# Kernel optimization log

Measured on AMD Instinct MI355X. Metric: run time of the kernel, lower is better.

## Reference

```python
import jax, jax.numpy as jnp
import numpy as np


def _prelu(x, a):
    return jnp.where(x >= 0, x, a * x)


def _conv1x1(x, w, b, a):
    # x: [N,C,H,W], w: [O,C], b: [O] -> PReLU(conv1x1(x))
    y = jnp.einsum('oc,nchw->nohw', w, x) + b[None, :, None, None]
    return _prelu(y, a)


def setup_inputs() -> dict:
    key = jax.random.key(0)
    ks = jax.random.split(key, 8)
    N, C, H, W = 4, 128, 64, 64
    Cr = C // 2  # reduction=2
    sC = 1.0 / np.sqrt(C)
    x = jax.random.normal(ks[0], (N, C, H, W), dtype=jnp.float32)
    w1 = jax.random.normal(ks[1], (Cr, C), dtype=jnp.float32) * sC
    b1 = jnp.zeros((Cr,), dtype=jnp.float32)
    a1 = jnp.asarray(0.25, dtype=jnp.float32)  # PReLU (single shared slope)
    w2 = jax.random.normal(ks[2], (Cr, C), dtype=jnp.float32) * sC
    b2 = jnp.zeros((Cr,), dtype=jnp.float32)
    a2 = jnp.asarray(0.25, dtype=jnp.float32)
    wa = jax.random.normal(ks[3], (C, C), dtype=jnp.float32) * sC
    ba = jnp.zeros((C,), dtype=jnp.float32)
    aa = jnp.asarray(0.25, dtype=jnp.float32)
    return {"x": x, "w1": w1, "b1": b1, "a1": a1,
            "w2": w2, "b2": b2, "a2": a2,
            "wa": wa, "ba": ba, "aa": aa}


def reference(x, w1, b1, a1, w2, b2, a2, wa, ba, aa):
    N, C, H, W = x.shape
    HW = H * W
    e1 = _conv1x1(x, w1, b1, a1).reshape(N, -1, HW)   # [N,Cr,HW]
    e2 = _conv1x1(x, w2, b2, a2).reshape(N, -1, HW)   # [N,Cr,HW]
    asm = _conv1x1(x, wa, ba, aa).reshape(N, C, HW)   # [N,C,HW]
    # ksize=1: per-channel outer products summed over channels == single contraction
    score = jnp.einsum('nci,ncj->nij', e1, e2)        # [N,HW,HW]
    score = jax.nn.softmax(score, axis=2)
    out = jnp.einsum('nij,ncj->nci', score, asm)      # [N,C,HW]
    return out.reshape(N, C, H, W)
```

## Files before the change

kernel.cpp:

```cpp
#include <hip/hip_runtime.h>
#include <hip/hip_bf16.h>
#include <stdint.h>


typedef float   f32x16 __attribute__((ext_vector_type(16)));
typedef __bf16  bf16x8 __attribute__((ext_vector_type(8)));
typedef __bf16  bf16x2 __attribute__((ext_vector_type(2)));
typedef unsigned int u32x4 __attribute__((ext_vector_type(4)));
typedef unsigned int u32x2 __attribute__((ext_vector_type(2)));

#define L2E 1.4426950408889634f

#define Q_OFF   (0u)
#define K_OFF   (2u << 20)
#define V_OFF   (4u << 20)
#define DEN_OFF (8u << 20)
#define WH_OFF  ((8u << 20) + (1u << 19))
#define WL_OFF  (WH_OFF + (1u << 16))
#define OP_OFF  (9u << 20)

__device__ inline unsigned short f2bf(float f) {
  unsigned u = __builtin_bit_cast(unsigned, f);
  return (unsigned short)((u + 0x7FFFu + ((u >> 16) & 1u)) >> 16);
}
__device__ inline float bf2f(unsigned short h) {
  unsigned u = ((unsigned)h) << 16;
  return __builtin_bit_cast(float, u);
}

__device__ inline void gld_lds16(const void* g, void* l) {
  __builtin_amdgcn_global_load_lds(
      (const __attribute__((address_space(1))) unsigned*)g,
      (__attribute__((address_space(3))) unsigned*)l, 16, 0, 0);
}

__global__ void wcast_kernel(const float* __restrict__ w1, const float* __restrict__ w2,
                             const float* __restrict__ wa, char* __restrict__ ws) {
  int idx = blockIdx.x * 256 + threadIdx.x;
  unsigned short* WH = (unsigned short*)(ws + WH_OFF);
  unsigned short* WL = (unsigned short*)(ws + WL_OFF);
#pragma unroll
  for (int r = 0; r < 4; ++r) {
    int i = r * 8192 + idx;
    int oc = i >> 7, c = i & 127;
    float v = oc < 64 ? w1[oc * 128 + c]
            : (oc < 128 ? w2[(oc - 64) * 128 + c] : wa[(oc - 128) * 128 + c]);
    unsigned short h = f2bf(v);
    WH[i] = h;
    WL[i] = f2bf(v - bf2f(h));
  }
}

__global__ __launch_bounds__(256) void conv_kernel(
    const float* __restrict__ x, char* __restrict__ ws,
    const float* __restrict__ b1, const float* __restrict__ a1,
    const float* __restrict__ b2, const float* __restrict__ a2,
    const float* __restrict__ ba, const float* __restrict__ aa) {
  int bid = blockIdx.x;
  int n = bid >> 7, st = bid & 127;
  int sb = st * 32;
  int tid = threadIdx.x;
  int wid = tid >> 6, lane = tid & 63, l31 = lane & 31, hi = lane >> 5;

  __shared__ float xl[128][36];
  __shared__ float tl[2][64][33];

  const float* xb = x + (size_t)n * 128 * 4096;
#pragma unroll
  for (int it = 0; it < 4; ++it) {
    int flat4 = tid + 256 * it;
    int c = flat4 >> 3, s4 = flat4 & 7;
    float4 v = *(const float4*)(xb + (size_t)c * 4096 + sb + s4 * 4);
    *(float4*)&xl[c][s4 * 4] = v;
  }
  __syncthreads();

  const char* WH = ws + WH_OFF;
  const char* WL = ws + WL_OFF;
  int oc0 = wid * 64;

  f32x16 acc[2];
  acc[0] = 0.f; acc[1] = 0.f;
#pragma unroll
  for (int c0 = 0; c0 < 8; ++c0) {
    __bf16 eh[8], el[8];
#pragma unroll
    for (int j = 0; j < 8; ++j) {
      float v = xl[c0 * 16 + hi * 8 + j][l31];
      __bf16 h = (__bf16)v;
      eh[j] = h;
      el[j] = (__bf16)(v - (float)h);
    }
    bf16x8 xh = {eh[0], eh[1], eh[2], eh[3], eh[4], eh[5], eh[6], eh[7]};
    bf16x8 xlo = {el[0], el[1], el[2], el[3], el[4], el[5], el[6], el[7]};
#pragma unroll
    for (int mb = 0; mb < 2; ++mb) {
      size_t wo = (size_t)(oc0 + mb * 32 + l31) * 256 + c0 * 32 + hi * 16;
      bf16x8 wh = *(const bf16x8*)(WH + wo);
      bf16x8 wl = *(const bf16x8*)(WL + wo);
      acc[mb] = __builtin_amdgcn_mfma_f32_32x32x16_bf16(wh, xh, acc[mb], 0, 0, 0);
      acc[mb] = __builtin_amdgcn_mfma_f32_32x32x16_bf16(wh, xlo, acc[mb], 0, 0, 0);
      acc[mb] = __builtin_amdgcn_mfma_f32_32x32x16_bf16(wl, xh, acc[mb], 0, 0, 0);
    }
  }

  char* Qw = ws + Q_OFF + (size_t)n * (4096 * 64 * 2);
  char* Kw = ws + K_OFF + (size_t)n * (4096 * 64 * 2);
  unsigned short* Vw = (unsigned short*)(ws + V_OFF) + (size_t)n * 128 * 4096;

  if (wid < 2) {
    const float* bb = wid ? b2 : b1;
    float slope = wid ? a2[0] : a1[0];
    float scl = wid ? 1.0f : L2E;
#pragma unroll
    for (int mb = 0; mb < 2; ++mb)
#pragma unroll
      for (int reg = 0; reg < 16; ++reg) {
        int row = mb * 32 + (reg & 3) + 8 * (reg >> 2) + 4 * hi;
        float y = acc[mb][reg] + bb[row];
        y = fmaxf(y, 0.f) + slope * fminf(y, 0.f);
        tl[wid][row][l31] = y * scl;
      }
  } else {
    float slope = aa[0];
#pragma unroll
    for (int mb = 0; mb < 2; ++mb)
#pragma unroll
      for (int reg = 0; reg < 16; ++reg) {
        int dv = (wid - 2) * 64 + mb * 32 + (reg & 3) + 8 * (reg >> 2) + 4 * hi;
        float y = acc[mb][reg] + ba[dv];
        y = fmaxf(y, 0.f) + slope * fminf(y, 0.f);
        Vw[(size_t)dv * 4096 + sb + l31] = f2bf(y);
      }
  }
  __syncthreads();
  if (wid < 2) {
    char* Og = wid ? Kw : Qw;
#pragma unroll
    for (int it = 0; it < 4; ++it) {
      int sl = (lane >> 3) + it * 8;
      unsigned short u[8];
#pragma unroll
      for (int i = 0; i < 8; ++i) u[i] = f2bf(tl[wid][(lane & 7) * 8 + i][sl]);
      u32x4 pv;
      pv.x = ((unsigned)u[1] << 16) | u[0]; pv.y = ((unsigned)u[3] << 16) | u[2];
      pv.z = ((unsigned)u[5] << 16) | u[4]; pv.w = ((unsigned)u[7] << 16) | u[6];
      *(u32x4*)(Og + (size_t)(sb + sl) * 128 + (lane & 7) * 16) = pv;
    }
  }
}

__global__ __launch_bounds__(256, 4) void attn_kernel(char* __restrict__ ws) {
  int bid = blockIdx.x;
  int split = bid & 7;
  int qt = (bid >> 3) & 31;
  int batch = bid >> 8;
  int tid = threadIdx.x;
  int wid = tid >> 6, lane = tid & 63, l31 = lane & 31, hi = lane >> 5;

  const char* Qb = ws + Q_OFF + (size_t)batch * (4096 * 64 * 2);
  const char* Kb = ws + K_OFF + (size_t)batch * (4096 * 64 * 2);
  const char* Vb = ws + V_OFF + (size_t)batch * (128 * 4096 * 2);

  __shared__ char kbuf[2][32 * 128];
  __shared__ char vbuf[2][128 * 64];

  int q0 = qt * 128 + wid * 32;

  bf16x8 qf[4];
#pragma unroll
  for (int d0 = 0; d0 < 4; ++d0)
    qf[d0] = *(const bf16x8*)(Qb + (size_t)(q0 + l31) * 128 + d0 * 32 + hi * 16);

  f32x16 oacc[4];
#pragma unroll
  for (int i = 0; i < 4; ++i) oacc[i] = 0.f;
  float den = 0.f;

  int t0 = split * 16;

  auto stage = [&](int b, int tile) {
    int kv0 = tile * 32;
    {
      int base = wid * 1024;
      int L = base + (lane << 4);
      int r = L >> 7, sl = (L >> 4) & 7;
      const char* src = Kb + (size_t)(kv0 + r) * 128 + ((sl ^ (r & 7)) << 4);
      gld_lds16(src, &kbuf[b][base]);
    }
#pragma unroll
    for (int i = 0; i < 2; ++i) {
      int base = wid * 2048 + i * 1024;
      int L = base + (lane << 4);
      int r = L >> 6, sl = (L >> 4) & 3;
      const char* src = Vb + (size_t)r * 8192 + kv0 * 2 + ((sl ^ (r & 3)) << 4);
      gld_lds16(src, &vbuf[b][base]);
    }
  };

  stage(0, t0);
  __syncthreads();
  int cur = 0;

  for (int t = 0; t < 16; ++t) {
    if (t + 1 < 16) stage(cur ^ 1, t0 + t + 1);

    f32x16 sacc;
    sacc = 0.f;
    __builtin_amdgcn_s_setprio(1);
#pragma unroll
    for (int d0 = 0; d0 < 4; ++d0) {
      int r = l31;
      bf16x8 kf = *(const bf16x8*)(
          &kbuf[cur][r * 128 + (((d0 * 2 + hi) ^ (r & 7)) << 4)]);
      sacc = __builtin_amdgcn_mfma_f32_32x32x16_bf16(kf, qf[d0], sacc, 0, 0, 0);
    }
    __builtin_amdgcn_s_setprio(0);

    unsigned pk[8];
#pragma unroll
    for (int m = 0; m < 8; ++m) {
      float e0 = __builtin_amdgcn_exp2f(sacc[2 * m]);
      float e1 = __builtin_amdgcn_exp2f(sacc[2 * m + 1]);
      den += e0 + e1;
      bf16x2 bp = { (__bf16)e0, (__bf16)e1 };
      pk[m] = __builtin_bit_cast(unsigned, bp);
    }

#pragma unroll
    for (int kc = 0; kc < 2; ++kc) {
      const int bs = kc * 4;
      u32x2 r0 = __builtin_amdgcn_permlane32_swap(pk[bs + 0], pk[bs + 2],
                                                  false, false);
      u32x2 r1 = __builtin_amdgcn_permlane32_swap(pk[bs + 1], pk[bs + 3],
                                                  false, false);
      u32x4 pu = {r0.x, r1.x, r0.y, r1.y};
      bf16x8 pf = __builtin_bit_cast(bf16x8, pu);
      __builtin_amdgcn_s_setprio(1);
#pragma unroll
      for (int dvb = 0; dvb < 4; ++dvb) {
        int r = dvb * 32 + l31;
        bf16x8 vf = *(const bf16x8*)(
            &vbuf[cur][r * 64 + (((kc * 2 + hi) ^ (r & 3)) << 4)]);
        oacc[dvb] = __builtin_amdgcn_mfma_f32_32x32x16_bf16(vf, pf,
                                                            oacc[dvb], 0, 0, 0);
      }
      __builtin_amdgcn_s_setprio(0);
    }

    __syncthreads();
    cur ^= 1;
  }

  unsigned short* OPu = (unsigned short*)(ws + OP_OFF) +
                        (size_t)((batch * 32 + qt) * 8 + split) * 128 * 128;
  int qloc = wid * 32 + l31;
#pragma unroll
  for (int dvb = 0; dvb < 4; ++dvb)
#pragma unroll
    for (int reg = 0; reg < 16; ++reg) {
      int dv = dvb * 32 + (reg & 3) + 8 * (reg >> 2) + 4 * hi;
      OPu[dv * 128 + qloc] = f2bf(oacc[dvb][reg]);
    }
  float dtot = den + __shfl_xor(den, 32, 64);
  if (hi == 0) {
    float* DEN = (float*)(ws + DEN_OFF) +
                 (size_t)((batch * 32 + qt) * 8 + split) * 128;
    DEN[qloc] = dtot;
  }
}

__global__ __launch_bounds__(256) void combine_kernel(const char* __restrict__ ws,
                                                      float* __restrict__ out) {
  int idx = blockIdx.x * 256 + threadIdx.x;
  int n = idx >> 19;
  int dv = (idx >> 12) & 127;
  int s = idx & 4095;
  int qt = s >> 7, ql = s & 127;
  const unsigned short* OPu = (const unsigned short*)(ws + OP_OFF);
  const float* DEN = (const float*)(ws + DEN_OFF);
  size_t pb = (size_t)((n * 32 + qt) * 8);
  float num = 0.f, den = 0.f;
#pragma unroll
  for (int h = 0; h < 8; ++h) {
    num += bf2f(OPu[(pb + h) * 16384 + (size_t)dv * 128 + ql]);
    den += DEN[(pb + h) * 128 + ql];
  }
  out[idx] = num / den;
}

extern "C" void kernel_launch(void* const* d_in, const int* in_sizes, int n_in,
                              void* d_out, int out_size, void* d_ws, size_t ws_size,
                              hipStream_t stream) {
  (void)in_sizes; (void)n_in; (void)out_size; (void)ws_size;
  const float* x  = (const float*)d_in[0];
  const float* w1 = (const float*)d_in[1];
  const float* b1 = (const float*)d_in[2];
  const float* a1 = (const float*)d_in[3];
  const float* w2 = (const float*)d_in[4];
  const float* b2 = (const float*)d_in[5];
  const float* a2 = (const float*)d_in[6];
  const float* wa = (const float*)d_in[7];
  const float* ba = (const float*)d_in[8];
  const float* aa = (const float*)d_in[9];
  char* ws = (char*)d_ws;
  float* out = (float*)d_out;

  wcast_kernel<<<dim3(32), dim3(256), 0, stream>>>(w1, w2, wa, ws);
  conv_kernel<<<dim3(512), dim3(256), 0, stream>>>(x, ws, b1, a1, b2, a2, ba, aa);
  attn_kernel<<<dim3(1024), dim3(256), 0, stream>>>(ws);
  combine_kernel<<<dim3(8192), dim3(256), 0, stream>>>(ws, out);
}
```

Measured before the change: 64.13 us.

## Vectorize combine kernel, pre-split x into bf16 LDS, use hardware bf16 conversion

The combine kernel now makes each thread handle 8 outputs with 16-byte bf16 and float4 loads and stores, and launches 8x fewer blocks. The conv kernel splits x into hi/lo bf16 parts once while staging it into transposed LDS tiles, so the inner loop does vector LDS reads instead of scalar reads plus per-iteration conversion. f2bf switches from manual round-to-nearest-even integer math to the native __bf16 cast, and a pack2 helper packs pairs of floats into bf16. The transposed LDS writes at element granularity may cause bank conflicts.

```diff
diff --git a/kernel.cpp b/kernel.cpp
--- a/kernel.cpp
+++ b/kernel.cpp
@@ -20,12 +20,16 @@
 #define OP_OFF  (9u << 20)
 
 __device__ inline unsigned short f2bf(float f) {
-  unsigned u = __builtin_bit_cast(unsigned, f);
-  return (unsigned short)((u + 0x7FFFu + ((u >> 16) & 1u)) >> 16);
+  __bf16 h = (__bf16)f;
+  return __builtin_bit_cast(unsigned short, h);
 }
 __device__ inline float bf2f(unsigned short h) {
   unsigned u = ((unsigned)h) << 16;
   return __builtin_bit_cast(float, u);
+}
+__device__ inline unsigned pack2(float a, float b) {
+  bf16x2 t = { (__bf16)a, (__bf16)b };
+  return __builtin_bit_cast(unsigned, t);
 }
 
 __device__ inline void gld_lds16(const void* g, void* l) {
@@ -45,9 +49,9 @@
     int oc = i >> 7, c = i & 127;
     float v = oc < 64 ? w1[oc * 128 + c]
             : (oc < 128 ? w2[(oc - 64) * 128 + c] : wa[(oc - 128) * 128 + c]);
-    unsigned short h = f2bf(v);
-    WH[i] = h;
-    WL[i] = f2bf(v - bf2f(h));
+    __bf16 h = (__bf16)v;
+    WH[i] = __builtin_bit_cast(unsigned short, h);
+    WL[i] = f2bf(v - (float)h);
   }
 }
 
@@ -62,7 +66,8 @@
   int tid = threadIdx.x;
   int wid = tid >> 6, lane = tid & 63, l31 = lane & 31, hi = lane >> 5;
 
-  __shared__ float xl[128][36];
+  __shared__ __bf16 xh[32][152];
+  __shared__ __bf16 xlo[32][152];
   __shared__ float tl[2][64][33];
 
   const float* xb = x + (size_t)n * 128 * 4096;
@@ -71,36 +76,38 @@
     int flat4 = tid + 256 * it;
     int c = flat4 >> 3, s4 = flat4 & 7;
     float4 v = *(const float4*)(xb + (size_t)c * 4096 + sb + s4 * 4);
-    *(float4*)&xl[c][s4 * 4] = v;
+    float vv[4] = {v.x, v.y, v.z, v.w};
+#pragma unroll
+    for (int e = 0; e < 4; ++e) {
+      int s = s4 * 4 + e;
+      __bf16 h = (__bf16)vv[e];
+      xh[s][c] = h;
+      xlo[s][c] = (__bf16)(vv[e] - (float)h);
+    }
   }
   __syncthreads();
 
   const char* WH = ws + WH_OFF;
   const char* WL = ws + WL_OFF;
+  const char* xhB = (const char*)&xh[0][0];
+  const char* xlB = (const char*)&xlo[0][0];
   int oc0 = wid * 64;
 
   f32x16 acc[2];
   acc[0] = 0.f; acc[1] = 0.f;
 #pragma unroll
   for (int c0 = 0; c0 < 8; ++c0) {
-    __bf16 eh[8], el[8];
-#pragma unroll
-    for (int j = 0; j < 8; ++j) {
-      float v = xl[c0 * 16 + hi * 8 + j][l31];
-      __bf16 h = (__bf16)v;
-      eh[j] = h;
-      el[j] = (__bf16)(v - (float)h);
-    }
-    bf16x8 xh = {eh[0], eh[1], eh[2], eh[3], eh[4], eh[5], eh[6], eh[7]};
-    bf16x8 xlo = {el[0], el[1], el[2], el[3], el[4], el[5], el[6], el[7]};
+    int xo = l31 * 304 + c0 * 32 + hi * 16;
+    bf16x8 xfh = *(const bf16x8*)(xhB + xo);
+    bf16x8 xfl = *(const bf16x8*)(xlB + xo);
 #pragma unroll
     for (int mb = 0; mb < 2; ++mb) {
       size_t wo = (size_t)(oc0 + mb * 32 + l31) * 256 + c0 * 32 + hi * 16;
       bf16x8 wh = *(const bf16x8*)(WH + wo);
       bf16x8 wl = *(const bf16x8*)(WL + wo);
-      acc[mb] = __builtin_amdgcn_mfma_f32_32x32x16_bf16(wh, xh, acc[mb], 0, 0, 0);
-      acc[mb] = __builtin_amdgcn_mfma_f32_32x32x16_bf16(wh, xlo, acc[mb], 0, 0, 0);
-      acc[mb] = __builtin_amdgcn_mfma_f32_32x32x16_bf16(wl, xh, acc[mb], 0, 0, 0);
+      acc[mb] = __builtin_amdgcn_mfma_f32_32x32x16_bf16(wh, xfh, acc[mb], 0, 0, 0);
+      acc[mb] = __builtin_amdgcn_mfma_f32_32x32x16_bf16(wh, xfl, acc[mb], 0, 0, 0);
+      acc[mb] = __builtin_amdgcn_mfma_f32_32x32x16_bf16(wl, xfh, acc[mb], 0, 0, 0);
     }
   }
 
@@ -139,12 +146,11 @@
 #pragma unroll
     for (int it = 0; it < 4; ++it) {
       int sl = (lane >> 3) + it * 8;
-      unsigned short u[8];
-#pragma unroll
-      for (int i = 0; i < 8; ++i) u[i] = f2bf(tl[wid][(lane & 7) * 8 + i][sl]);
       u32x4 pv;
-      pv.x = ((unsigned)u[1] << 16) | u[0]; pv.y = ((unsigned)u[3] << 16) | u[2];
-      pv.z = ((unsigned)u[5] << 16) | u[4]; pv.w = ((unsigned)u[7] << 16) | u[6];
+#pragma unroll
+      for (int p = 0; p < 4; ++p)
+        pv[p] = pack2(tl[wid][(lane & 7) * 8 + 2 * p][sl],
+                      tl[wid][(lane & 7) * 8 + 2 * p + 1][sl]);
       *(u32x4*)(Og + (size_t)(sb + sl) * 128 + (lane & 7) * 16) = pv;
     }
   }
@@ -223,8 +229,7 @@
       float e0 = __builtin_amdgcn_exp2f(sacc[2 * m]);
       float e1 = __builtin_amdgcn_exp2f(sacc[2 * m + 1]);
       den += e0 + e1;
-      bf16x2 bp = { (__bf16)e0, (__bf16)e1 };
-      pk[m] = __builtin_bit_cast(unsigned, bp);
+      pk[m] = pack2(e0, e1);
     }
 
 #pragma unroll
@@ -253,7 +258,7 @@
   }
 
   unsigned short* OPu = (unsigned short*)(ws + OP_OFF) +
-                        (size_t)((batch * 32 + qt) * 8 + split) * 128 * 128;
+                        (size_t)((batch * 32 + qt) * 8 + split) * 16384;
   int qloc = wid * 32 + l31;
 #pragma unroll
   for (int dvb = 0; dvb < 4; ++dvb)
@@ -272,21 +277,32 @@
 
 __global__ __launch_bounds__(256) void combine_kernel(const char* __restrict__ ws,
                                                       float* __restrict__ out) {
-  int idx = blockIdx.x * 256 + threadIdx.x;
-  int n = idx >> 19;
-  int dv = (idx >> 12) & 127;
-  int s = idx & 4095;
-  int qt = s >> 7, ql = s & 127;
+  int idx8 = (blockIdx.x * 256 + threadIdx.x) * 8;
+  int n = idx8 >> 19;
+  int dv = (idx8 >> 12) & 127;
+  int s0 = idx8 & 4095;
+  int qt = s0 >> 7, ql = s0 & 127;
   const unsigned short* OPu = (const unsigned short*)(ws + OP_OFF);
   const float* DEN = (const float*)(ws + DEN_OFF);
   size_t pb = (size_t)((n * 32 + qt) * 8);
-  float num = 0.f, den = 0.f;
+  float num[8], den[8];
+#pragma unroll
+  for (int j = 0; j < 8; ++j) { num[j] = 0.f; den[j] = 0.f; }
 #pragma unroll
   for (int h = 0; h < 8; ++h) {
-    num += bf2f(OPu[(pb + h) * 16384 + (size_t)dv * 128 + ql]);
-    den += DEN[(pb + h) * 128 + ql];
-  }
-  out[idx] = num / den;
+    bf16x8 v = *(const bf16x8*)(OPu + (pb + h) * 16384 + (size_t)dv * 128 + ql);
+    const float* dp = DEN + (pb + h) * 128 + ql;
+    float4 d0 = *(const float4*)dp;
+    float4 d1 = *(const float4*)(dp + 4);
+#pragma unroll
+    for (int j = 0; j < 8; ++j) num[j] += (float)v[j];
+    den[0] += d0.x; den[1] += d0.y; den[2] += d0.z; den[3] += d0.w;
+    den[4] += d1.x; den[5] += d1.y; den[6] += d1.z; den[7] += d1.w;
+  }
+  float4 o0 = {num[0] / den[0], num[1] / den[1], num[2] / den[2], num[3] / den[3]};
+  float4 o1 = {num[4] / den[4], num[5] / den[5], num[6] / den[6], num[7] / den[7]};
+  *(float4*)&out[idx8] = o0;
+  *(float4*)&out[idx8 + 4] = o1;
 }
 
 extern "C" void kernel_launch(void* const* d_in, const int* in_sizes, int n_in,
@@ -309,5 +325,5 @@
   wcast_kernel<<<dim3(32), dim3(256), 0, stream>>>(w1, w2, wa, ws);
   conv_kernel<<<dim3(512), dim3(256), 0, stream>>>(x, ws, b1, a1, b2, a2, ba, aa);
   attn_kernel<<<dim3(1024), dim3(256), 0, stream>>>(ws);
-  combine_kernel<<<dim3(8192), dim3(256), 0, stream>>>(ws, out);
-}
+  combine_kernel<<<dim3(1024), dim3(256), 0, stream>>>(ws, out);
+}
```

Result: slower. 66.88 us (+4.3%).
